# Kernel tuning notes

Hardware: AMD Instinct MI355X
Metric: run time of the kernel (lower is better)

The kernel has to match this reference:

```python
import jax, jax.numpy as jnp
import numpy as np

EPS = 1e-5

def _bn_train(h, gamma, beta):
    # BatchNorm1d in training mode: batch mean and biased variance over batch dim
    mu = jnp.mean(h, axis=0)
    var = jnp.mean((h - mu) ** 2, axis=0)
    return (h - mu) * jax.lax.rsqrt(var + EPS) * gamma + beta

def setup_inputs() -> dict:
    key = jax.random.key(0)
    ks = jax.random.split(key, 12)
    B, IN, H1, H2, NC = 16384, 4096, 256, 128, 12
    x = jax.random.normal(ks[0], (B, 1, 64, 64), dtype=jnp.float32)
    y = jax.random.randint(ks[1], (B,), 0, NC, dtype=jnp.int32)
    s1 = 1.0 / np.sqrt(IN)
    W1 = jax.random.uniform(ks[2], (H1, IN), jnp.float32, -s1, s1)
    b1 = jax.random.uniform(ks[3], (H1,), jnp.float32, -s1, s1)
    g1 = jax.random.normal(ks[4], (H1,), jnp.float32) * 0.1 + 1.0
    be1 = jax.random.normal(ks[5], (H1,), jnp.float32) * 0.1
    s2 = 1.0 / np.sqrt(H1)
    W2 = jax.random.uniform(ks[6], (H2, H1), jnp.float32, -s2, s2)
    b2 = jax.random.uniform(ks[7], (H2,), jnp.float32, -s2, s2)
    g2 = jax.random.normal(ks[8], (H2,), jnp.float32) * 0.1 + 1.0
    be2 = jax.random.normal(ks[9], (H2,), jnp.float32) * 0.1
    s4 = 1.0 / np.sqrt(H2)
    W4 = jax.random.uniform(ks[10], (NC, H2), jnp.float32, -s4, s4)
    b4 = jax.random.uniform(ks[11], (NC,), jnp.float32, -s4, s4)
    return {"x": x, "W1": W1, "b1": b1, "g1": g1, "be1": be1,
            "W2": W2, "b2": b2, "g2": g2, "be2": be2,
            "W4": W4, "b4": b4, "y": y}

def reference(x, W1, b1, g1, be1, W2, b2, g2, be2, W4, b4, y):
    B = x.shape[0]
    h = x.reshape(B, -1)  # [B, 4096]
    # layer 1: binarized linear + BN(train) + hardtanh (dropout p=0 is identity)
    h = h @ jnp.sign(W1).T + jnp.sign(b1)
    h = jnp.clip(_bn_train(h, g1, be1), -1.0, 1.0)
    # layer 2
    h = h @ jnp.sign(W2).T + jnp.sign(b2)
    h = jnp.clip(_bn_train(h, g2, be2), -1.0, 1.0)
    # final float linear
    return h @ W4.T + b4  # [B, 12]
```

## Files before the change

kernel.cpp:

```cpp
#include <hip/hip_runtime.h>
#include <cstddef>

typedef __attribute__((ext_vector_type(8))) short short8;
typedef __attribute__((ext_vector_type(4))) float f4;
typedef __attribute__((ext_vector_type(4))) unsigned int u4;

__device__ __forceinline__ unsigned int f2bf(float f){
  unsigned int u = __float_as_uint(f);
  u += 0x7fffu + ((u >> 16) & 1u);
  return u >> 16;
}
__device__ __forceinline__ float fsign(float x){ return (x > 0.f) ? 1.f : ((x < 0.f) ? -1.f : 0.f); }
__device__ __forceinline__ float hclip(float x){ return fminf(1.f, fmaxf(-1.f, x)); }

#define BARRIER() do { \
    __builtin_amdgcn_sched_barrier(0); \
    asm volatile("s_waitcnt lgkmcnt(0)" ::: "memory"); \
    __builtin_amdgcn_s_barrier(); \
    asm volatile("" ::: "memory"); \
    __builtin_amdgcn_sched_barrier(0); \
  } while(0)

__global__ void prep_sign_k(const float* __restrict__ W1, unsigned short* __restrict__ w1s,
                            const float* __restrict__ W2, unsigned short* __restrict__ w2s){
  int i = (blockIdx.x * blockDim.x + threadIdx.x) * 8;
  const float* w; unsigned short* o; int off;
  if (i < 1048576){ w = W1; o = w1s; off = i; }
  else            { w = W2; o = w2s; off = i - 1048576; if (off >= 32768) return; }
  f4 a = *(const f4*)(w + off);
  f4 b = *(const f4*)(w + off + 4);
  unsigned short s[8];
  #pragma unroll
  for (int j = 0; j < 4; j++) s[j]   = (a[j] > 0.f) ? 0x3F80u : ((a[j] < 0.f) ? 0xBF80u : 0u);
  #pragma unroll
  for (int j = 0; j < 4; j++) s[4+j] = (b[j] > 0.f) ? 0x3F80u : ((b[j] < 0.f) ? 0xBF80u : 0u);
  u4 v;
  v.x = (unsigned)s[0] | ((unsigned)s[1] << 16);
  v.y = (unsigned)s[2] | ((unsigned)s[3] << 16);
  v.z = (unsigned)s[4] | ((unsigned)s[5] << 16);
  v.w = (unsigned)s[6] | ((unsigned)s[7] << 16);
  *(u4*)(o + off) = v;
}

__global__ __launch_bounds__(512) void gemm1_k(
    const float* __restrict__ x, const unsigned short* __restrict__ w1s,
    const float* __restrict__ b1, unsigned short* __restrict__ h1,
    float* __restrict__ part1s, float* __restrict__ part1q)
{
  __shared__ __align__(16) char lds[16384];
  const int tid  = threadIdx.x;
  const int lane = tid & 63;
  const int wid  = tid >> 6;
  const int cl   = lane & 15;
  const int g    = lane >> 4;
  const int klo  = g * 8;
  const int row0 = blockIdx.x * 64;

  const int am  = tid >> 3;
  const int ak0 = (tid & 7) * 8;
  const float* xA = x + (size_t)(row0 + am) * 4096 + ak0;
  const int aoff  = ((am * 128) + (ak0 * 2)) ^ ((am & 7) << 4);

  const unsigned short* wbase = w1s + (size_t)(wid * 32 + cl) * 4096 + klo;

  f4 acc[4][2];
  const f4 z = {0.f, 0.f, 0.f, 0.f};
  #pragma unroll
  for (int i = 0; i < 4; i++){ acc[i][0] = z; acc[i][1] = z; }

  f4 ra0a, ra0b, ra1a, ra1b, ra2a, ra2b, ra3a, ra3b;
  short8 bq0, bq1, bq2, bq3, br0, br1, br2, br3;

#define LOADT(S, KB) do { \
    ra##S##a = *(const f4*)(xA + (KB)*64); \
    ra##S##b = *(const f4*)(xA + (KB)*64 + 4); \
  } while(0)

#define LOADB(P, KB) do { \
    b##P##0 = *(const short8*)(wbase + (KB)*64); \
    b##P##1 = *(const short8*)(wbase + (KB)*64 + 32); \
    b##P##2 = *(const short8*)(wbase + 65536 + (KB)*64); \
    b##P##3 = *(const short8*)(wbase + 65536 + (KB)*64 + 32); \
  } while(0)

#define WRITET(S, BUF) do { \
    u4 _va; \
    _va.x = f2bf(ra##S##a[0]) | (f2bf(ra##S##a[1]) << 16); \
    _va.y = f2bf(ra##S##a[2]) | (f2bf(ra##S##a[3]) << 16); \
    _va.z = f2bf(ra##S##b[0]) | (f2bf(ra##S##b[1]) << 16); \
    _va.w = f2bf(ra##S##b[2]) | (f2bf(ra##S##b[3]) << 16); \
    *(u4*)(lds + (BUF)*8192 + aoff) = _va; \
  } while(0)

#define COMPUTE(P, BUF) do { \
    const char* _ab = lds + (BUF)*8192; \
    short8 _af[4][2]; \
    _Pragma("unroll") \
    for (int fm = 0; fm < 4; fm++){ \
      int _m = fm*16 + cl; \
      _af[fm][0] = *(const short8*)(_ab + ((_m*128 + klo*2) ^ ((_m & 7) << 4))); \
      _af[fm][1] = *(const short8*)(_ab + ((_m*128 + (32 + klo)*2) ^ ((_m & 7) << 4))); \
    } \
    _Pragma("unroll") \
    for (int fm = 0; fm < 4; fm++){ \
      acc[fm][0] = __builtin_amdgcn_mfma_f32_16x16x32_bf16(_af[fm][0], b##P##0, acc[fm][0], 0, 0, 0); \
      acc[fm][1] = __builtin_amdgcn_mfma_f32_16x16x32_bf16(_af[fm][0], b##P##2, acc[fm][1], 0, 0, 0); \
      acc[fm][0] = __builtin_amdgcn_mfma_f32_16x16x32_bf16(_af[fm][1], b##P##1, acc[fm][0], 0, 0, 0); \
      acc[fm][1] = __builtin_amdgcn_mfma_f32_16x16x32_bf16(_af[fm][1], b##P##3, acc[fm][1], 0, 0, 0); \
    } \
  } while(0)

  LOADB(q, 0);
  LOADT(0, 0); LOADT(1, 1); LOADT(2, 2);
  WRITET(0, 0);
  BARRIER();
  for (int t = 0; t < 64; t += 4){
    LOADB(r, t+1);
    COMPUTE(q, 0);
    __builtin_amdgcn_sched_barrier(0);
    LOADT(3, t+3);
    __builtin_amdgcn_sched_barrier(0);
    WRITET(1, 1);
    BARRIER();
    LOADB(q, t+2);
    COMPUTE(r, 1);
    __builtin_amdgcn_sched_barrier(0);
    if (t+4 < 64) LOADT(0, t+4);
    __builtin_amdgcn_sched_barrier(0);
    WRITET(2, 0);
    BARRIER();
    LOADB(r, t+3);
    COMPUTE(q, 0);
    __builtin_amdgcn_sched_barrier(0);
    if (t+5 < 64) LOADT(1, t+5);
    __builtin_amdgcn_sched_barrier(0);
    WRITET(3, 1);
    BARRIER();
    if (t+4 < 64) LOADB(q, t+4);
    COMPUTE(r, 1);
    __builtin_amdgcn_sched_barrier(0);
    if (t+6 < 64) LOADT(2, t+6);
    __builtin_amdgcn_sched_barrier(0);
    if (t+4 < 64) WRITET(0, 0);
    BARRIER();
  }
#undef COMPUTE
#undef WRITET
#undef LOADB
#undef LOADT

  #pragma unroll
  for (int fn = 0; fn < 2; fn++){
    int c = wid*32 + fn*16 + cl;
    float sb = fsign(b1[c]);
    float s = 0.f, q = 0.f;
    #pragma unroll
    for (int fm = 0; fm < 4; fm++){
      int rbase = row0 + fm*16 + g*4;
      #pragma unroll
      for (int i = 0; i < 4; i++){
        float v = acc[fm][fn][i] + sb;
        h1[(size_t)(rbase + i)*256 + c] = (unsigned short)f2bf(v);
        s += v; q += v*v;
      }
    }
    s += __shfl_xor(s, 16, 64); s += __shfl_xor(s, 32, 64);
    q += __shfl_xor(q, 16, 64); q += __shfl_xor(q, 32, 64);
    if (g == 0){
      part1s[c*256 + blockIdx.x] = s;
      part1q[c*256 + blockIdx.x] = q;
    }
  }
}

template<int COLS>
__global__ __launch_bounds__(64) void params_k(
    const float* __restrict__ ps, const float* __restrict__ pq,
    const float* __restrict__ g, const float* __restrict__ be,
    float* __restrict__ ab){
  int j = blockIdx.x * 64 + threadIdx.x;
  const f4* vs = (const f4*)(ps + j*256);
  const f4* vq = (const f4*)(pq + j*256);
  f4 s4 = {0,0,0,0}, q4 = {0,0,0,0};
  #pragma unroll 8
  for (int b = 0; b < 64; b++){ s4 += vs[b]; q4 += vq[b]; }
  float s = s4[0]+s4[1]+s4[2]+s4[3];
  float q = q4[0]+q4[1]+q4[2]+q4[3];
  float mu  = s * (1.f/16384.f);
  float var = q * (1.f/16384.f) - mu*mu;
  float a   = g[j] * rsqrtf(var + 1e-5f);
  ab[j] = a;
  ab[COLS + j] = be[j] - mu*a;
}

__global__ __launch_bounds__(512) void gemm2_k(
    const unsigned short* __restrict__ h1, const unsigned short* __restrict__ w2s,
    const float* __restrict__ b2, const float* __restrict__ ab1,
    unsigned short* __restrict__ h2, float* __restrict__ part2s, float* __restrict__ part2q)
{
  __shared__ __align__(16) char lds[16384];
  __shared__ __align__(16) float a1l[256];
  __shared__ __align__(16) float c1l[256];
  const int tid  = threadIdx.x;
  const int lane = tid & 63;
  const int wid  = tid >> 6;
  const int cl   = lane & 15;
  const int g    = lane >> 4;
  const int klo  = g * 8;
  const int row0 = blockIdx.x * 64;

  if (tid < 256) a1l[tid] = ab1[tid];
  else           c1l[tid - 256] = ab1[tid];

  const int am  = tid >> 3;
  const int ak0 = (tid & 7) * 8;
  const unsigned short* hA = h1 + (size_t)(row0 + am) * 256 + ak0;
  const int aw = ((am * 128) + (ak0 * 2)) ^ ((am & 7) << 4);

  const unsigned short* wbase = w2s + (size_t)(wid * 16 + cl) * 256 + klo;

  f4 acc[4];
  const f4 z = {0.f, 0.f, 0.f, 0.f};
  #pragma unroll
  for (int i = 0; i < 4; i++) acc[i] = z;

  auto writeA = [&](int buf, int kb, u4 raw){
    f4 a0 = *(const f4*)&a1l[kb*64 + ak0];
    f4 a1 = *(const f4*)&a1l[kb*64 + ak0 + 4];
    f4 c0 = *(const f4*)&c1l[kb*64 + ak0];
    f4 c1 = *(const f4*)&c1l[kb*64 + ak0 + 4];
    float t0 = hclip(a0[0]*__uint_as_float((raw.x & 0xFFFFu) << 16) + c0[0]);
    float t1 = hclip(a0[1]*__uint_as_float( raw.x & 0xFFFF0000u   ) + c0[1]);
    float t2 = hclip(a0[2]*__uint_as_float((raw.y & 0xFFFFu) << 16) + c0[2]);
    float t3 = hclip(a0[3]*__uint_as_float( raw.y & 0xFFFF0000u   ) + c0[3]);
    float t4 = hclip(a1[0]*__uint_as_float((raw.z & 0xFFFFu) << 16) + c1[0]);
    float t5 = hclip(a1[1]*__uint_as_float( raw.z & 0xFFFF0000u   ) + c1[1]);
    float t6 = hclip(a1[2]*__uint_as_float((raw.w & 0xFFFFu) << 16) + c1[2]);
    float t7 = hclip(a1[3]*__uint_as_float( raw.w & 0xFFFF0000u   ) + c1[3]);
    u4 v;
    v.x = f2bf(t0) | (f2bf(t1) << 16);
    v.y = f2bf(t2) | (f2bf(t3) << 16);
    v.z = f2bf(t4) | (f2bf(t5) << 16);
    v.w = f2bf(t6) | (f2bf(t7) << 16);
    *(u4*)(lds + buf*8192 + aw) = v;
  };
  auto compute = [&](int buf, int kb){
    short8 bf[2];
    #pragma unroll
    for (int ks = 0; ks < 2; ks++)
      bf[ks] = *(const short8*)(wbase + kb*64 + ks*32);
    const char* abuf = lds + buf*8192;
    short8 af[4][2];
    #pragma unroll
    for (int fm = 0; fm < 4; fm++){
      int m = fm*16 + cl;
      #pragma unroll
      for (int ks = 0; ks < 2; ks++){
        int off = (m*128 + (ks*32 + klo)*2) ^ ((m & 7) << 4);
        af[fm][ks] = *(const short8*)(abuf + off);
      }
    }
    #pragma unroll
    for (int ks = 0; ks < 2; ks++)
      #pragma unroll
      for (int fm = 0; fm < 4; fm++)
        acc[fm] = __builtin_amdgcn_mfma_f32_16x16x32_bf16(af[fm][ks], bf[ks], acc[fm], 0, 0, 0);
  };

  u4 raw0 = *(const u4*)(hA);
  BARRIER();
  writeA(0, 0, raw0);
  BARRIER();
  #pragma unroll
  for (int kb = 0; kb < 4; kb++){
    u4 rawn;
    if (kb < 3) rawn = *(const u4*)(hA + (kb+1)*64);
    compute(kb & 1, kb);
    if (kb < 3) writeA((kb+1) & 1, kb+1, rawn);
    BARRIER();
  }

  {
    int c = wid*16 + cl;
    float sb = fsign(b2[c]);
    float s = 0.f, q = 0.f;
    #pragma unroll
    for (int fm = 0; fm < 4; fm++){
      int rbase = row0 + fm*16 + g*4;
      #pragma unroll
      for (int i = 0; i < 4; i++){
        float v = acc[fm][i] + sb;
        h2[(size_t)(rbase + i)*128 + c] = (unsigned short)f2bf(v);
        s += v; q += v*v;
      }
    }
    s += __shfl_xor(s, 16, 64); s += __shfl_xor(s, 32, 64);
    q += __shfl_xor(q, 16, 64); q += __shfl_xor(q, 32, 64);
    if (g == 0){
      part2s[c*256 + blockIdx.x] = s;
      part2q[c*256 + blockIdx.x] = q;
    }
  }
}

__global__ __launch_bounds__(64) void final_k(
    const unsigned short* __restrict__ h2, const float* __restrict__ ab2,
    const float* __restrict__ W4, const float* __restrict__ b4,
    float* __restrict__ out)
{
  __shared__ __align__(16) float W4l[12*128];
  __shared__ __align__(16) float a2l[128];
  __shared__ __align__(16) float c2l[128];
  const int t = threadIdx.x;
  #pragma unroll
  for (int i = 0; i < 6; i++)
    *(f4*)&W4l[(i*64 + t)*4] = *(const f4*)(W4 + (i*64 + t)*4);
  a2l[t]      = ab2[t];
  a2l[t + 64] = ab2[t + 64];
  c2l[t]      = ab2[128 + t];
  c2l[t + 64] = ab2[192 + t];
  __syncthreads();

  const int r = blockIdx.x * 64 + t;
  const u4* hp = (const u4*)(h2 + (size_t)r * 128);
  u4 hv0 = hp[0], hv1 = hp[1], hv2 = hp[2],  hv3 = hp[3];
  u4 hv4 = hp[4], hv5 = hp[5], hv6 = hp[6],  hv7 = hp[7];
  u4 hv8 = hp[8], hv9 = hp[9], hv10 = hp[10], hv11 = hp[11];
  u4 hv12 = hp[12], hv13 = hp[13], hv14 = hp[14], hv15 = hp[15];

  float acc[12];
  #pragma unroll
  for (int o = 0; o < 12; o++) acc[o] = b4[o];

#define FPROC(HV, J) do { \
    f4 a0 = *(const f4*)&a2l[(J)*8];     f4 a1 = *(const f4*)&a2l[(J)*8 + 4]; \
    f4 c0 = *(const f4*)&c2l[(J)*8];     f4 c1 = *(const f4*)&c2l[(J)*8 + 4]; \
    float tt0 = hclip(a0[0]*__uint_as_float((HV.x & 0xFFFFu) << 16) + c0[0]); \
    float tt1 = hclip(a0[1]*__uint_as_float( HV.x & 0xFFFF0000u   ) + c0[1]); \
    float tt2 = hclip(a0[2]*__uint_as_float((HV.y & 0xFFFFu) << 16) + c0[2]); \
    float tt3 = hclip(a0[3]*__uint_as_float( HV.y & 0xFFFF0000u   ) + c0[3]); \
    float tt4 = hclip(a1[0]*__uint_as_float((HV.z & 0xFFFFu) << 16) + c1[0]); \
    float tt5 = hclip(a1[1]*__uint_as_float( HV.z & 0xFFFF0000u   ) + c1[1]); \
    float tt6 = hclip(a1[2]*__uint_as_float((HV.w & 0xFFFFu) << 16) + c1[2]); \
    float tt7 = hclip(a1[3]*__uint_as_float( HV.w & 0xFFFF0000u   ) + c1[3]); \
    _Pragma("unroll") \
    for (int o = 0; o < 12; o++){ \
      f4 w0 = *(const f4*)&W4l[o*128 + (J)*8]; \
      f4 w1 = *(const f4*)&W4l[o*128 + (J)*8 + 4]; \
      acc[o] += tt0*w0[0] + tt1*w0[1] + tt2*w0[2] + tt3*w0[3] \
              + tt4*w1[0] + tt5*w1[1] + tt6*w1[2] + tt7*w1[3]; \
    } \
  } while(0)

  FPROC(hv0, 0);  FPROC(hv1, 1);  FPROC(hv2, 2);   FPROC(hv3, 3);
  FPROC(hv4, 4);  FPROC(hv5, 5);  FPROC(hv6, 6);   FPROC(hv7, 7);
  FPROC(hv8, 8);  FPROC(hv9, 9);  FPROC(hv10, 10); FPROC(hv11, 11);
  FPROC(hv12, 12); FPROC(hv13, 13); FPROC(hv14, 14); FPROC(hv15, 15);
#undef FPROC

  #pragma unroll
  for (int o = 0; o < 12; o++) out[(size_t)r*12 + o] = acc[o];
}

extern "C" void kernel_launch(void* const* d_in, const int* in_sizes, int n_in,
                              void* d_out, int out_size, void* d_ws, size_t ws_size,
                              hipStream_t stream)
{
  const float* x   = (const float*)d_in[0];
  const float* W1  = (const float*)d_in[1];
  const float* b1  = (const float*)d_in[2];
  const float* g1  = (const float*)d_in[3];
  const float* be1 = (const float*)d_in[4];
  const float* W2  = (const float*)d_in[5];
  const float* b2  = (const float*)d_in[6];
  const float* g2  = (const float*)d_in[7];
  const float* be2 = (const float*)d_in[8];
  const float* W4  = (const float*)d_in[9];
  const float* b4  = (const float*)d_in[10];
  float* out = (float*)d_out;

  char* ws = (char*)d_ws;
  unsigned short* h1     = (unsigned short*)(ws);
  unsigned short* h2     = (unsigned short*)(ws + 8388608);
  unsigned short* w1s    = (unsigned short*)(ws + 12582912);
  unsigned short* w2s    = (unsigned short*)(ws + 14680064);
  float*          part1s = (float*)(ws + 14745600);
  float*          part1q = (float*)(ws + 15007744);
  float*          part2s = (float*)(ws + 15269888);
  float*          part2q = (float*)(ws + 15400960);
  float*          ab1    = (float*)(ws + 15532032);
  float*          ab2    = (float*)(ws + 15534080);

  prep_sign_k<<<528, 256, 0, stream>>>(W1, w1s, W2, w2s);
  gemm1_k<<<256, 512, 0, stream>>>(x, w1s, b1, h1, part1s, part1q);
  params_k<256><<<4, 64, 0, stream>>>(part1s, part1q, g1, be1, ab1);
  gemm2_k<<<256, 512, 0, stream>>>(h1, w2s, b2, ab1, h2, part2s, part2q);
  params_k<128><<<2, 64, 0, stream>>>(part2s, part2q, g2, be2, ab2);
  final_k<<<256, 64, 0, stream>>>(h2, ab2, W4, b4, out);
}
```

Baseline: 126.0 us.

## Stage four K-slices per barrier in gemm1 and preload whole A tile in gemm2

gemm1 now loads four 64-wide K slices of x at once and converts them to bf16 into a 32KB half of a 64KB double-buffered LDS region. This cuts the number of barriers per block from 64 to 16. gemm2 loads all four A slices up front, applies the BN1 affine and clip, stages them in LDS, and runs the four MFMA steps with a single barrier, reading ab1 straight from global memory instead of copying it into LDS first. The larger LDS footprint (64KB per block in gemm1) may lower occupancy and raises register pressure from holding more prefetched data.

Result: no change. 125.5 us (-0.4%).

```diff
diff --git a/kernel.cpp b/kernel.cpp
--- a/kernel.cpp
+++ b/kernel.cpp
@@ -10,6 +10,8 @@
   u += 0x7fffu + ((u >> 16) & 1u);
   return u >> 16;
 }
+__device__ __forceinline__ float bflo(unsigned int w){ return __uint_as_float((w & 0xFFFFu) << 16); }
+__device__ __forceinline__ float bfhi(unsigned int w){ return __uint_as_float(w & 0xFFFF0000u); }
 __device__ __forceinline__ float fsign(float x){ return (x > 0.f) ? 1.f : ((x < 0.f) ? -1.f : 0.f); }
 __device__ __forceinline__ float hclip(float x){ return fminf(1.f, fmaxf(-1.f, x)); }
 
@@ -47,7 +49,7 @@
     const float* __restrict__ b1, unsigned short* __restrict__ h1,
     float* __restrict__ part1s, float* __restrict__ part1q)
 {
-  __shared__ __align__(16) char lds[16384];
+  __shared__ __align__(16) char lds[65536];
   const int tid  = threadIdx.x;
   const int lane = tid & 63;
   const int wid  = tid >> 6;
@@ -68,32 +70,41 @@
   #pragma unroll
   for (int i = 0; i < 4; i++){ acc[i][0] = z; acc[i][1] = z; }
 
-  f4 ra0a, ra0b, ra1a, ra1b, ra2a, ra2b, ra3a, ra3b;
-  short8 bq0, bq1, bq2, bq3, br0, br1, br2, br3;
-
-#define LOADT(S, KB) do { \
-    ra##S##a = *(const f4*)(xA + (KB)*64); \
-    ra##S##b = *(const f4*)(xA + (KB)*64 + 4); \
+  f4 rA0a, rA0b, rA1a, rA1b, rA2a, rA2b, rA3a, rA3b;
+  short8 Bq0, Bq1, Bq2, Bq3, Br0, Br1, Br2, Br3;
+
+#define LOADA4(KB0) do { \
+    rA0a = *(const f4*)(xA + (KB0+0)*64); rA0b = *(const f4*)(xA + (KB0+0)*64 + 4); \
+    rA1a = *(const f4*)(xA + (KB0+1)*64); rA1b = *(const f4*)(xA + (KB0+1)*64 + 4); \
+    rA2a = *(const f4*)(xA + (KB0+2)*64); rA2b = *(const f4*)(xA + (KB0+2)*64 + 4); \
+    rA3a = *(const f4*)(xA + (KB0+3)*64); rA3b = *(const f4*)(xA + (KB0+3)*64 + 4); \
+  } while(0)
+
+#define PACK1(DST, RA, RB) do { \
+    u4 _v; \
+    _v.x = f2bf(RA[0]) | (f2bf(RA[1]) << 16); \
+    _v.y = f2bf(RA[2]) | (f2bf(RA[3]) << 16); \
+    _v.z = f2bf(RB[0]) | (f2bf(RB[1]) << 16); \
+    _v.w = f2bf(RB[2]) | (f2bf(RB[3]) << 16); \
+    *(u4*)(DST) = _v; \
+  } while(0)
+
+#define WRITEA4(WB) do { \
+    PACK1((WB) +     0 + aoff, rA0a, rA0b); \
+    PACK1((WB) +  8192 + aoff, rA1a, rA1b); \
+    PACK1((WB) + 16384 + aoff, rA2a, rA2b); \
+    PACK1((WB) + 24576 + aoff, rA3a, rA3b); \
   } while(0)
 
 #define LOADB(P, KB) do { \
-    b##P##0 = *(const short8*)(wbase + (KB)*64); \
-    b##P##1 = *(const short8*)(wbase + (KB)*64 + 32); \
-    b##P##2 = *(const short8*)(wbase + 65536 + (KB)*64); \
-    b##P##3 = *(const short8*)(wbase + 65536 + (KB)*64 + 32); \
-  } while(0)
-
-#define WRITET(S, BUF) do { \
-    u4 _va; \
-    _va.x = f2bf(ra##S##a[0]) | (f2bf(ra##S##a[1]) << 16); \
-    _va.y = f2bf(ra##S##a[2]) | (f2bf(ra##S##a[3]) << 16); \
-    _va.z = f2bf(ra##S##b[0]) | (f2bf(ra##S##b[1]) << 16); \
-    _va.w = f2bf(ra##S##b[2]) | (f2bf(ra##S##b[3]) << 16); \
-    *(u4*)(lds + (BUF)*8192 + aoff) = _va; \
-  } while(0)
-
-#define COMPUTE(P, BUF) do { \
-    const char* _ab = lds + (BUF)*8192; \
+    B##P##0 = *(const short8*)(wbase + (KB)*64); \
+    B##P##1 = *(const short8*)(wbase + (KB)*64 + 32); \
+    B##P##2 = *(const short8*)(wbase + 65536 + (KB)*64); \
+    B##P##3 = *(const short8*)(wbase + 65536 + (KB)*64 + 32); \
+  } while(0)
+
+#define COMPUTE(BASE, P) do { \
+    const char* _ab = (const char*)(BASE); \
     short8 _af[4][2]; \
     _Pragma("unroll") \
     for (int fm = 0; fm < 4; fm++){ \
@@ -103,51 +114,41 @@
     } \
     _Pragma("unroll") \
     for (int fm = 0; fm < 4; fm++){ \
-      acc[fm][0] = __builtin_amdgcn_mfma_f32_16x16x32_bf16(_af[fm][0], b##P##0, acc[fm][0], 0, 0, 0); \
-      acc[fm][1] = __builtin_amdgcn_mfma_f32_16x16x32_bf16(_af[fm][0], b##P##2, acc[fm][1], 0, 0, 0); \
-      acc[fm][0] = __builtin_amdgcn_mfma_f32_16x16x32_bf16(_af[fm][1], b##P##1, acc[fm][0], 0, 0, 0); \
-      acc[fm][1] = __builtin_amdgcn_mfma_f32_16x16x32_bf16(_af[fm][1], b##P##3, acc[fm][1], 0, 0, 0); \
+      acc[fm][0] = __builtin_amdgcn_mfma_f32_16x16x32_bf16(_af[fm][0], B##P##0, acc[fm][0], 0, 0, 0); \
+      acc[fm][1] = __builtin_amdgcn_mfma_f32_16x16x32_bf16(_af[fm][0], B##P##2, acc[fm][1], 0, 0, 0); \
+      acc[fm][0] = __builtin_amdgcn_mfma_f32_16x16x32_bf16(_af[fm][1], B##P##1, acc[fm][0], 0, 0, 0); \
+      acc[fm][1] = __builtin_amdgcn_mfma_f32_16x16x32_bf16(_af[fm][1], B##P##3, acc[fm][1], 0, 0, 0); \
     } \
   } while(0)
 
+  LOADA4(0);
+  WRITEA4(lds);
   LOADB(q, 0);
-  LOADT(0, 0); LOADT(1, 1); LOADT(2, 2);
-  WRITET(0, 0);
   BARRIER();
-  for (int t = 0; t < 64; t += 4){
-    LOADB(r, t+1);
-    COMPUTE(q, 0);
+
+  for (int p = 0; p < 16; ++p){
+    const bool pg = (p < 15);
+    char* rbuf = lds + ((p & 1) << 15);
+    char* wbuf = lds + (((p & 1) ^ 1) << 15);
+    if (pg) LOADA4(4*p + 4);
     __builtin_amdgcn_sched_barrier(0);
-    LOADT(3, t+3);
+    LOADB(r, 4*p + 1);
+    COMPUTE(rbuf,         q);
+    LOADB(q, 4*p + 2);
+    COMPUTE(rbuf +  8192, r);
+    LOADB(r, 4*p + 3);
+    COMPUTE(rbuf + 16384, q);
+    if (pg) LOADB(q, 4*p + 4);
+    COMPUTE(rbuf + 24576, r);
     __builtin_amdgcn_sched_barrier(0);
-    WRITET(1, 1);
-    BARRIER();
-    LOADB(q, t+2);
-    COMPUTE(r, 1);
-    __builtin_amdgcn_sched_barrier(0);
-    if (t+4 < 64) LOADT(0, t+4);
-    __builtin_amdgcn_sched_barrier(0);
-    WRITET(2, 0);
-    BARRIER();
-    LOADB(r, t+3);
-    COMPUTE(q, 0);
-    __builtin_amdgcn_sched_barrier(0);
-    if (t+5 < 64) LOADT(1, t+5);
-    __builtin_amdgcn_sched_barrier(0);
-    WRITET(3, 1);
-    BARRIER();
-    if (t+4 < 64) LOADB(q, t+4);
-    COMPUTE(r, 1);
-    __builtin_amdgcn_sched_barrier(0);
-    if (t+6 < 64) LOADT(2, t+6);
-    __builtin_amdgcn_sched_barrier(0);
-    if (t+4 < 64) WRITET(0, 0);
+    if (pg) WRITEA4(wbuf);
     BARRIER();
   }
 #undef COMPUTE
-#undef WRITET
 #undef LOADB
-#undef LOADT
+#undef WRITEA4
+#undef PACK1
+#undef LOADA4
 
   #pragma unroll
   for (int fn = 0; fn < 2; fn++){
@@ -198,9 +199,7 @@
     const float* __restrict__ b2, const float* __restrict__ ab1,
     unsigned short* __restrict__ h2, float* __restrict__ part2s, float* __restrict__ part2q)
 {
-  __shared__ __align__(16) char lds[16384];
-  __shared__ __align__(16) float a1l[256];
-  __shared__ __align__(16) float c1l[256];
+  __shared__ __align__(16) char lds[32768];
   const int tid  = threadIdx.x;
   const int lane = tid & 63;
   const int wid  = tid >> 6;
@@ -209,76 +208,80 @@
   const int klo  = g * 8;
   const int row0 = blockIdx.x * 64;
 
-  if (tid < 256) a1l[tid] = ab1[tid];
-  else           c1l[tid - 256] = ab1[tid];
-
   const int am  = tid >> 3;
   const int ak0 = (tid & 7) * 8;
   const unsigned short* hA = h1 + (size_t)(row0 + am) * 256 + ak0;
   const int aw = ((am * 128) + (ak0 * 2)) ^ ((am & 7) << 4);
-
   const unsigned short* wbase = w2s + (size_t)(wid * 16 + cl) * 256 + klo;
+
+  u4 q0 = *(const u4*)(hA);
+  u4 q1 = *(const u4*)(hA + 64);
+  u4 q2 = *(const u4*)(hA + 128);
+  u4 q3 = *(const u4*)(hA + 192);
+  short8 Bq0, Bq1, Br0, Br1;
+  Bq0 = *(const short8*)(wbase);
+  Bq1 = *(const short8*)(wbase + 32);
+
+#define TRW(KB, RAW) do { \
+    f4 _a0 = *(const f4*)(ab1 + (KB)*64 + ak0); \
+    f4 _a1 = *(const f4*)(ab1 + (KB)*64 + ak0 + 4); \
+    f4 _c0 = *(const f4*)(ab1 + 256 + (KB)*64 + ak0); \
+    f4 _c1 = *(const f4*)(ab1 + 256 + (KB)*64 + ak0 + 4); \
+    float _t0 = hclip(_a0[0]*bflo(RAW.x) + _c0[0]); \
+    float _t1 = hclip(_a0[1]*bfhi(RAW.x) + _c0[1]); \
+    float _t2 = hclip(_a0[2]*bflo(RAW.y) + _c0[2]); \
+    float _t3 = hclip(_a0[3]*bfhi(RAW.y) + _c0[3]); \
+    float _t4 = hclip(_a1[0]*bflo(RAW.z) + _c1[0]); \
+    float _t5 = hclip(_a1[1]*bfhi(RAW.z) + _c1[1]); \
+    float _t6 = hclip(_a1[2]*bflo(RAW.w) + _c1[2]); \
+    float _t7 = hclip(_a1[3]*bfhi(RAW.w) + _c1[3]); \
+    u4 _v; \
+    _v.x = f2bf(_t0) | (f2bf(_t1) << 16); \
+    _v.y = f2bf(_t2) | (f2bf(_t3) << 16); \
+    _v.z = f2bf(_t4) | (f2bf(_t5) << 16); \
+    _v.w = f2bf(_t6) | (f2bf(_t7) << 16); \
+    *(u4*)(lds + (KB)*8192 + aw) = _v; \
+  } while(0)
+
+  TRW(0, q0); TRW(1, q1); TRW(2, q2); TRW(3, q3);
+#undef TRW
+  BARRIER();
 
   f4 acc[4];
   const f4 z = {0.f, 0.f, 0.f, 0.f};
   #pragma unroll
   for (int i = 0; i < 4; i++) acc[i] = z;
 
-  auto writeA = [&](int buf, int kb, u4 raw){
-    f4 a0 = *(const f4*)&a1l[kb*64 + ak0];
-    f4 a1 = *(const f4*)&a1l[kb*64 + ak0 + 4];
-    f4 c0 = *(const f4*)&c1l[kb*64 + ak0];
-    f4 c1 = *(const f4*)&c1l[kb*64 + ak0 + 4];
-    float t0 = hclip(a0[0]*__uint_as_float((raw.x & 0xFFFFu) << 16) + c0[0]);
-    float t1 = hclip(a0[1]*__uint_as_float( raw.x & 0xFFFF0000u   ) + c0[1]);
-    float t2 = hclip(a0[2]*__uint_as_float((raw.y & 0xFFFFu) << 16) + c0[2]);
-    float t3 = hclip(a0[3]*__uint_as_float( raw.y & 0xFFFF0000u   ) + c0[3]);
-    float t4 = hclip(a1[0]*__uint_as_float((raw.z & 0xFFFFu) << 16) + c1[0]);
-    float t5 = hclip(a1[1]*__uint_as_float( raw.z & 0xFFFF0000u   ) + c1[1]);
-    float t6 = hclip(a1[2]*__uint_as_float((raw.w & 0xFFFFu) << 16) + c1[2]);
-    float t7 = hclip(a1[3]*__uint_as_float( raw.w & 0xFFFF0000u   ) + c1[3]);
-    u4 v;
-    v.x = f2bf(t0) | (f2bf(t1) << 16);
-    v.y = f2bf(t2) | (f2bf(t3) << 16);
-    v.z = f2bf(t4) | (f2bf(t5) << 16);
-    v.w = f2bf(t6) | (f2bf(t7) << 16);
-    *(u4*)(lds + buf*8192 + aw) = v;
-  };
-  auto compute = [&](int buf, int kb){
-    short8 bf[2];
-    #pragma unroll
-    for (int ks = 0; ks < 2; ks++)
-      bf[ks] = *(const short8*)(wbase + kb*64 + ks*32);
-    const char* abuf = lds + buf*8192;
-    short8 af[4][2];
-    #pragma unroll
-    for (int fm = 0; fm < 4; fm++){
-      int m = fm*16 + cl;
-      #pragma unroll
-      for (int ks = 0; ks < 2; ks++){
-        int off = (m*128 + (ks*32 + klo)*2) ^ ((m & 7) << 4);
-        af[fm][ks] = *(const short8*)(abuf + off);
-      }
-    }
-    #pragma unroll
-    for (int ks = 0; ks < 2; ks++)
-      #pragma unroll
-      for (int fm = 0; fm < 4; fm++)
-        acc[fm] = __builtin_amdgcn_mfma_f32_16x16x32_bf16(af[fm][ks], bf[ks], acc[fm], 0, 0, 0);
-  };
-
-  u4 raw0 = *(const u4*)(hA);
-  BARRIER();
-  writeA(0, 0, raw0);
-  BARRIER();
-  #pragma unroll
-  for (int kb = 0; kb < 4; kb++){
-    u4 rawn;
-    if (kb < 3) rawn = *(const u4*)(hA + (kb+1)*64);
-    compute(kb & 1, kb);
-    if (kb < 3) writeA((kb+1) & 1, kb+1, rawn);
-    BARRIER();
-  }
+#define LOADB2(P, KB) do { \
+    B##P##0 = *(const short8*)(wbase + (KB)*64); \
+    B##P##1 = *(const short8*)(wbase + (KB)*64 + 32); \
+  } while(0)
+
+#define COMP2(BASE, P) do { \
+    const char* _ab = (const char*)(BASE); \
+    short8 _af[4][2]; \
+    _Pragma("unroll") \
+    for (int fm = 0; fm < 4; fm++){ \
+      int _m = fm*16 + cl; \
+      _af[fm][0] = *(const short8*)(_ab + ((_m*128 + klo*2) ^ ((_m & 7) << 4))); \
+      _af[fm][1] = *(const short8*)(_ab + ((_m*128 + (32 + klo)*2) ^ ((_m & 7) << 4))); \
+    } \
+    _Pragma("unroll") \
+    for (int fm = 0; fm < 4; fm++){ \
+      acc[fm] = __builtin_amdgcn_mfma_f32_16x16x32_bf16(_af[fm][0], B##P##0, acc[fm], 0, 0, 0); \
+      acc[fm] = __builtin_amdgcn_mfma_f32_16x16x32_bf16(_af[fm][1], B##P##1, acc[fm], 0, 0, 0); \
+    } \
+  } while(0)
+
+  LOADB2(r, 1);
+  COMP2(lds,         q);
+  LOADB2(q, 2);
+  COMP2(lds +  8192, r);
+  LOADB2(r, 3);
+  COMP2(lds + 16384, q);
+  COMP2(lds + 24576, r);
+#undef COMP2
+#undef LOADB2
 
   {
     int c = wid*16 + cl;
@@ -335,14 +338,14 @@
 #define FPROC(HV, J) do { \
     f4 a0 = *(const f4*)&a2l[(J)*8];     f4 a1 = *(const f4*)&a2l[(J)*8 + 4]; \
     f4 c0 = *(const f4*)&c2l[(J)*8];     f4 c1 = *(const f4*)&c2l[(J)*8 + 4]; \
-    float tt0 = hclip(a0[0]*__uint_as_float((HV.x & 0xFFFFu) << 16) + c0[0]); \
-    float tt1 = hclip(a0[1]*__uint_as_float( HV.x & 0xFFFF0000u   ) + c0[1]); \
-    float tt2 = hclip(a0[2]*__uint_as_float((HV.y & 0xFFFFu) << 16) + c0[2]); \
-    float tt3 = hclip(a0[3]*__uint_as_float( HV.y & 0xFFFF0000u   ) + c0[3]); \
-    float tt4 = hclip(a1[0]*__uint_as_float((HV.z & 0xFFFFu) << 16) + c1[0]); \
-    float tt5 = hclip(a1[1]*__uint_as_float( HV.z & 0xFFFF0000u   ) + c1[1]); \
-    float tt6 = hclip(a1[2]*__uint_as_float((HV.w & 0xFFFFu) << 16) + c1[2]); \
-    float tt7 = hclip(a1[3]*__uint_as_float( HV.w & 0xFFFF0000u   ) + c1[3]); \
+    float tt0 = hclip(a0[0]*bflo(HV.x) + c0[0]); \
+    float tt1 = hclip(a0[1]*bfhi(HV.x) + c0[1]); \
+    float tt2 = hclip(a0[2]*bflo(HV.y) + c0[2]); \
+    float tt3 = hclip(a0[3]*bfhi(HV.y) + c0[3]); \
+    float tt4 = hclip(a1[0]*bflo(HV.z) + c1[0]); \
+    float tt5 = hclip(a1[1]*bfhi(HV.z) + c1[1]); \
+    float tt6 = hclip(a1[2]*bflo(HV.w) + c1[2]); \
+    float tt7 = hclip(a1[3]*bfhi(HV.w) + c1[3]); \
     _Pragma("unroll") \
     for (int o = 0; o < 12; o++){ \
       f4 w0 = *(const f4*)&W4l[o*128 + (J)*8]; \
```
